# Kernel optimization log

Hardware: AMD Instinct MI355X
Metric: run time of the kernel (lower is better)

Reference implementation:

```python
import jax, jax.numpy as jnp
import numpy as np

K_ORDER, NUM_HEADS, BETA = 4, 2, 0.5
D_IN, D_OUT = 64, 64


def _batch_and_pos(n_nodes, N):
    # batch[i] = graph id of node i; pos[i] = index of node i within its graph
    batch = jnp.repeat(jnp.arange(n_nodes.shape[0], dtype=jnp.int32), n_nodes, total_repeat_length=N)
    ptr = jnp.concatenate([jnp.zeros(1, jnp.int32), jnp.cumsum(n_nodes).astype(jnp.int32)])
    pos = jnp.arange(N, dtype=jnp.int32) - ptr[batch]
    return batch, pos


def _to_pad(feat, batch, pos, Bsz, max_node):
    out_shape = (Bsz, max_node) + feat.shape[1:]
    return jnp.zeros(out_shape, feat.dtype).at[batch, pos].set(feat)


def fast_attn_conv(qs, ks, vs, n_nodes, batch, pos, max_node):
    # qs/ks/vs: [N,H,D]; linear attention with per-graph kv outer-product sums
    Bsz = n_nodes.shape[0]
    q_pad = _to_pad(qs, batch, pos, Bsz, max_node)  # [B,M,H,D]
    k_pad = _to_pad(ks, batch, pos, Bsz, max_node)
    v_pad = _to_pad(vs, batch, pos, Bsz, max_node)
    kv = jnp.einsum('bnhd,bnhe->bdhe', k_pad, v_pad)  # [B,D,H,D]
    v_sum = jax.ops.segment_sum(vs, batch, num_segments=Bsz)  # [B,H,D]
    k_sum = jax.ops.segment_sum(ks, batch, num_segments=Bsz)  # [B,H,D]
    numerator = jnp.einsum('bnhd,bdhe->bnhe', q_pad, kv)[batch, pos] + v_sum[batch]
    denom = jnp.einsum('bnhd,bhd->bnh', q_pad, k_sum)[batch, pos]
    denom = denom + n_nodes.astype(qs.dtype)[batch][:, None]
    return numerator / denom[..., None]


def gcn_conv(x, edge_index, e_feat):
    # x: [N,H,D], e_feat: [E,D]
    N = x.shape[0]
    row, col = edge_index[0], edge_index[1]
    deg = jax.ops.segment_sum(jnp.ones(row.shape[0], x.dtype), row, num_segments=N)
    dis = jnp.where(deg > 0, deg ** -0.5, jnp.zeros_like(deg))
    w = dis[row] * dis[col]  # [E]
    msg_edge = jax.ops.segment_sum(w[:, None] * e_feat, row, num_segments=N)  # [N,D]
    new_feat = jax.ops.segment_sum(x[col] * w[:, None, None], row, num_segments=N)  # [N,H,D]
    return new_feat + msg_edge[:, None, :]


def setup_inputs():
    key = jax.random.key(0)
    ks = jax.random.split(key, 10)
    B = 64
    n_nodes_np = np.tile(np.array([1000, 2000], np.int32), B // 2)  # sums to 96000
    N = int(n_nodes_np.sum())
    E = 768000
    x = jax.random.normal(ks[0], (N, D_IN), jnp.float32)
    edge_index = jax.random.randint(ks[1], (2, E), 0, N, jnp.int32)
    edge_attr = jax.random.randint(ks[2], (E, 3), 0, 8, jnp.int32)
    s = 0.02
    Wq_w = jax.random.normal(ks[3], (D_IN * NUM_HEADS, D_IN), jnp.float32) * s
    Wq_b = jnp.zeros((D_IN * NUM_HEADS,), jnp.float32)
    Wk_w = jax.random.normal(ks[4], (D_IN * NUM_HEADS, D_IN), jnp.float32) * s
    Wk_b = jnp.zeros((D_IN * NUM_HEADS,), jnp.float32)
    Wo_w = jax.random.normal(ks[5], (D_OUT, D_IN * NUM_HEADS), jnp.float32) * s
    Wo_b = jnp.zeros((D_OUT,), jnp.float32)
    bond_emb = jax.random.normal(ks[6], (3, 8, D_OUT), jnp.float32) * s
    return {"x": x, "Wq_w": Wq_w, "Wq_b": Wq_b, "Wk_w": Wk_w, "Wk_b": Wk_b,
            "Wo_w": Wo_w, "Wo_b": Wo_b, "bond_emb": bond_emb,
            "edge_index": edge_index, "edge_attr": edge_attr,
            "n_nodes": jnp.asarray(n_nodes_np)}


def reference(x, Wq_w, Wq_b, Wk_w, Wk_b, Wo_w, Wo_b, bond_emb, edge_index, edge_attr, n_nodes):
    N = x.shape[0]
    max_node = 2000  # static max over n_nodes
    batch, pos = _batch_and_pos(n_nodes, N)
    query = (x @ Wq_w.T + Wq_b).reshape(N, NUM_HEADS, D_IN)
    key_t = (x @ Wk_w.T + Wk_b).reshape(N, NUM_HEADS, D_IN)
    qs = query / jnp.linalg.norm(query, axis=2, keepdims=True)
    kk = key_t / jnp.linalg.norm(key_t, axis=2, keepdims=True)
    # BondEncoder: sum of per-feature embeddings
    e_feat = bond_emb[0][edge_attr[:, 0]] + bond_emb[1][edge_attr[:, 1]] + bond_emb[2][edge_attr[:, 2]]
    h = jnp.broadcast_to(x[:, None, :], (N, NUM_HEADS, D_IN))
    acc = h
    cur = h
    for _ in range(K_ORDER):
        gcn_i = gcn_conv(cur, edge_index, e_feat)
        attn_i = fast_attn_conv(qs, kk, cur, n_nodes, batch, pos, max_node)
        cur = BETA * gcn_i + (1.0 - BETA) * attn_i
        acc = acc + cur
    out = acc.reshape(N, NUM_HEADS * D_IN)
    return (out @ Wo_w.T + Wo_b) / NUM_HEADS
```

## Files before the change

kernel.cpp:

```cpp
#include <hip/hip_runtime.h>
#include <hip/hip_bf16.h>


typedef __attribute__((ext_vector_type(8))) short bf16x8;
typedef __attribute__((ext_vector_type(4))) float f32x4v;

#define CHUNK 50

__device__ __forceinline__ float asf(unsigned int u) { union { unsigned int i; float f; } v; v.i = u; return v.f; }
__device__ __forceinline__ float b2f_u(unsigned short u) { return asf((unsigned int)u << 16); }
__device__ __forceinline__ unsigned short f2b_u(float f) {
    __hip_bfloat16 h = __float2bfloat16(f);
    union { __hip_bfloat16 h; unsigned short u; } v; v.h = h; return v.u;
}
__device__ __forceinline__ unsigned int pack2(float a, float b) {
    return (unsigned int)f2b_u(a) | ((unsigned int)f2b_u(b) << 16);
}
__device__ __forceinline__ float wave_reduce_sum(float v) {
    #pragma unroll
    for (int off = 32; off > 0; off >>= 1) v += __shfl_xor(v, off, 64);
    return v;
}

__global__ void k_ptr(const int* __restrict__ nn, int* __restrict__ ptr,
                      int* __restrict__ cptr, int* __restrict__ tptr, int B) {
    if (threadIdx.x == 0 && blockIdx.x == 0) {
        int s = 0, c = 0, t = 0; ptr[0] = 0; cptr[0] = 0; tptr[0] = 0;
        for (int i = 0; i < B; ++i) {
            s += nn[i]; ptr[i + 1] = s;
            c += (nn[i] + CHUNK - 1) / CHUNK; cptr[i + 1] = c;
            t += (nn[i] + 15) / 16; tptr[i + 1] = t;
        }
    }
}

__global__ void k_batch(const int* __restrict__ ptr, int* __restrict__ batch) {
    int b = blockIdx.x;
    int s = ptr[b], e = ptr[b + 1];
    for (int i = s + threadIdx.x; i < e; i += blockDim.x) batch[i] = b;
}

__global__ void k_wcvt(const float* __restrict__ Wq_w, const float* __restrict__ Wk_w,
                       const float* __restrict__ Wo_w, unsigned short* __restrict__ Wb) {
    int i = blockIdx.x * 256 + threadIdx.x;
    if (i < 24576) {
        float v = (i < 8192) ? Wq_w[i] : ((i < 16384) ? Wk_w[i - 8192] : Wo_w[i - 16384]);
        Wb[i] = f2b_u(v);
    }
}

__global__ __launch_bounds__(256) void k_qkm(
    const float* __restrict__ x, const unsigned short* __restrict__ Wb,
    const float* __restrict__ Wq_b, const float* __restrict__ Wk_b,
    unsigned short* __restrict__ q, unsigned short* __restrict__ kq,
    unsigned short* __restrict__ curA, int N)
{
    int w = threadIdx.x >> 6, l = threadIdx.x & 63;
    int six = l & 15, quad = l >> 4;
    int base = (blockIdx.x * 4 + w) * 16;
    if (base >= N) return;
    int n = base + six;
    int nc = min(n, N - 1);

    const float* xr = x + (size_t)nc * 64;
    float4 xa = *(const float4*)(xr + quad * 8);
    float4 xb = *(const float4*)(xr + quad * 8 + 4);
    float4 xc = *(const float4*)(xr + 32 + quad * 8);
    float4 xd = *(const float4*)(xr + 32 + quad * 8 + 4);
    union { bf16x8 v; unsigned int u[4]; } b0, b1;
    b0.u[0] = pack2(xa.x, xa.y); b0.u[1] = pack2(xa.z, xa.w);
    b0.u[2] = pack2(xb.x, xb.y); b0.u[3] = pack2(xb.z, xb.w);
    b1.u[0] = pack2(xc.x, xc.y); b1.u[1] = pack2(xc.z, xc.w);
    b1.u[2] = pack2(xd.x, xd.y); b1.u[3] = pack2(xd.z, xd.w);
    if (n < N) {
        unsigned short* cr = curA + (size_t)n * 128;
        *(uint4*)(cr + quad * 8)       = make_uint4(b0.u[0], b0.u[1], b0.u[2], b0.u[3]);
        *(uint4*)(cr + 32 + quad * 8)  = make_uint4(b1.u[0], b1.u[1], b1.u[2], b1.u[3]);
        *(uint4*)(cr + 64 + quad * 8)  = make_uint4(b0.u[0], b0.u[1], b0.u[2], b0.u[3]);
        *(uint4*)(cr + 96 + quad * 8)  = make_uint4(b1.u[0], b1.u[1], b1.u[2], b1.u[3]);
    }

    #pragma unroll
    for (int g = 0; g < 4; ++g) {
        f32x4v c[4];
        #pragma unroll
        for (int tt = 0; tt < 4; ++tt) {
            int t = g * 4 + tt;
            const unsigned short* wr = Wb + (size_t)(t * 16 + six) * 64;
            bf16x8 a0 = *(const bf16x8*)(wr + quad * 8);
            bf16x8 a1 = *(const bf16x8*)(wr + 32 + quad * 8);
            f32x4v cc = {0.f, 0.f, 0.f, 0.f};
            cc = __builtin_amdgcn_mfma_f32_16x16x32_bf16(a0, b0.v, cc, 0, 0, 0);
            cc = __builtin_amdgcn_mfma_f32_16x16x32_bf16(a1, b1.v, cc, 0, 0, 0);
            c[tt] = cc;
        }
        const float* bias = (g < 2) ? Wq_b : Wk_b;
        int cb = (g & 1) * 64 + quad * 4;
        float ss = 0.f;
        #pragma unroll
        for (int tt = 0; tt < 4; ++tt)
            #pragma unroll
            for (int r = 0; r < 4; ++r) {
                float v = c[tt][r] + bias[cb + tt * 16 + r];
                c[tt][r] = v;
                ss += v * v;
            }
        ss += __shfl_xor(ss, 16, 64);
        ss += __shfl_xor(ss, 32, 64);
        float sc = rsqrtf(ss);
        if (n < N) {
            unsigned short* dst = ((g < 2) ? q : kq) + (size_t)n * 128;
            #pragma unroll
            for (int tt = 0; tt < 4; ++tt) {
                unsigned int u0 = pack2(c[tt][0] * sc, c[tt][1] * sc);
                unsigned int u1 = pack2(c[tt][2] * sc, c[tt][3] * sc);
                *(uint2*)(dst + cb + tt * 16) = make_uint2(u0, u1);
            }
        }
    }
}

__global__ void k_deg(const int* __restrict__ row, int* __restrict__ deg,
                      int* __restrict__ slot, int E) {
    int e = blockIdx.x * 256 + threadIdx.x;
    if (e < E) slot[e] = atomicAdd(&deg[row[e]], 1);
}

__global__ void k_scan1(const int* __restrict__ deg, int* __restrict__ rowstart,
                        int* __restrict__ bsum, float* __restrict__ dis, int N) {
    __shared__ int sh[256];
    int t = threadIdx.x, n = blockIdx.x * 256 + t;
    int v = (n < N) ? deg[n] : 0;
    if (n < N) dis[n] = v > 0 ? rsqrtf((float)v) : 0.f;
    sh[t] = v; __syncthreads();
    #pragma unroll
    for (int off = 1; off < 256; off <<= 1) {
        int add = (t >= off) ? sh[t - off] : 0;
        __syncthreads();
        sh[t] += add;
        __syncthreads();
    }
    if (n < N) rowstart[n] = sh[t] - v;
    if (t == 255) bsum[blockIdx.x] = sh[255];
}

__global__ void k_scan2(int* __restrict__ bsum, int nb) {
    __shared__ int sh[512];
    __shared__ int carry;
    int t = threadIdx.x;
    if (t == 0) carry = 0;
    __syncthreads();
    for (int base = 0; base < nb; base += 512) {
        int idx = base + t;
        int v = (idx < nb) ? bsum[idx] : 0;
        sh[t] = v; __syncthreads();
        for (int off = 1; off < 512; off <<= 1) {
            int add = (t >= off) ? sh[t - off] : 0;
            __syncthreads();
            sh[t] += add;
            __syncthreads();
        }
        if (idx < nb) bsum[idx] = sh[t] - v + carry;
        __syncthreads();
        if (t == 0) carry += sh[511];
        __syncthreads();
    }
}

__global__ void k_scan3(int* __restrict__ rowstart, const int* __restrict__ bsum, int N, int E) {
    int n = blockIdx.x * 256 + threadIdx.x;
    if (n < N) rowstart[n] += bsum[blockIdx.x];
    if (n == 0) rowstart[N] = E;
}

__global__ void k_fill(const int* __restrict__ eidx, const float* __restrict__ dis,
                       const int* __restrict__ rowstart, const int* __restrict__ slot,
                       int4* __restrict__ csr_pack, const int* __restrict__ eattr, int E) {
    int e = blockIdx.x * 256 + threadIdx.x;
    if (e >= E) return;
    int r = eidx[e], c = eidx[E + e];
    float wv = dis[r] * dis[c];
    int a0 = eattr[e * 3 + 0], a1 = eattr[e * 3 + 1], a2 = eattr[e * 3 + 2];
    int idx = rowstart[r] + slot[e];
    int4 v;
    v.x = c;
    v.y = __float_as_int(wv);
    v.z = a0 | (a1 << 8) | (a2 << 16);
    v.w = 0;
    csr_pack[idx] = v;
}

__global__ __launch_bounds__(256) void k_msg(
    const int* __restrict__ rowstart, const int4* __restrict__ csr_pack,
    const float* __restrict__ bond, unsigned short* __restrict__ msgb, int N) {
    __shared__ float bl[1536];
    int t = threadIdx.x, w = t >> 6, l = t & 63;
    for (int i = t; i < 1536; i += 256) bl[i] = bond[i];
    __syncthreads();
    for (int n = blockIdx.x * 4 + w; n < N; n += gridDim.x * 4) {
        int s0 = rowstart[n], s1 = rowstart[n + 1];
        float m = 0.f;
        #pragma unroll 4
        for (int i = s0; i < s1; ++i) {
            int4 pk = csr_pack[i];
            float wv = __int_as_float(pk.y);
            int att = pk.z;
            m += wv * (bl[(att & 255) * 64 + l] + bl[(8 + ((att >> 8) & 255)) * 64 + l]
                     + bl[(16 + (att >> 16)) * 64 + l]);
        }
        msgb[(size_t)n * 64 + l] = f2b_u(m);
    }
}

__global__ __launch_bounds__(256) void k_ksump(
    const unsigned short* __restrict__ kq, const int* __restrict__ ptr,
    const int* __restrict__ cptr, float* __restrict__ partKS, int B)
{
    int cid = blockIdx.x;
    if (cid >= cptr[B]) return;
    int lo = 0, hi = B - 1;
    while (lo < hi) { int mid = (lo + hi + 1) >> 1; if (cptr[mid] <= cid) lo = mid; else hi = mid - 1; }
    int b = lo;
    int start = ptr[b] + (cid - cptr[b]) * CHUNK;
    int end = min(start + CHUNK, ptr[b + 1]);
    int t = threadIdx.x, r = t >> 7, col = t & 127;
    float a = 0.f;
    for (int n = start + r; n < end; n += 2)
        a += b2f_u(kq[(size_t)n * 128 + col]);
    __shared__ float sh[256];
    sh[t] = a;
    __syncthreads();
    if (t < 128) partKS[(size_t)cid * 128 + t] = sh[t] + sh[t + 128];
}

__global__ __launch_bounds__(128) void k_ksr(
    const float* __restrict__ partKS, const int* __restrict__ cptr,
    float* __restrict__ ksum, int B)
{
    int b = blockIdx.x, t = threadIdx.x;
    float s = 0.f;
    int c0 = cptr[b], c1 = cptr[b + 1];
    for (int c = c0; c < c1; ++c) s += partKS[(size_t)c * 128 + t];
    ksum[b * 128 + t] = s;
}

__global__ __launch_bounds__(256) void k_denom(
    const unsigned short* __restrict__ q, const float* __restrict__ ksum,
    const int* __restrict__ batch, const int* __restrict__ nn,
    float* __restrict__ denom, int N)
{
    int w = threadIdx.x >> 6, l = threadIdx.x & 63;
    int n = blockIdx.x * 4 + w;
    if (n >= N) return;
    int b = batch[n];
    float d0 = b2f_u(q[(size_t)n * 128 + l]) * ksum[b * 128 + l];
    float d1 = b2f_u(q[(size_t)n * 128 + 64 + l]) * ksum[b * 128 + 64 + l];
    d0 = wave_reduce_sum(d0);
    d1 = wave_reduce_sum(d1);
    if (l == 0) {
        float nf = (float)nn[b];
        denom[n * 2 + 0] = d0 + nf;
        denom[n * 2 + 1] = d1 + nf;
    }
}

__global__ __launch_bounds__(256) void k_kvp(
    const unsigned short* __restrict__ kq, const unsigned short* __restrict__ cur,
    const int* __restrict__ ptr, const int* __restrict__ cptr,
    unsigned short* __restrict__ partKV, float* __restrict__ partVS, int B)
{
    int cid = blockIdx.x;
    if (cid >= cptr[B]) return;
    int lo = 0, hi = B - 1;
    while (lo < hi) { int mid = (lo + hi + 1) >> 1; if (cptr[mid] <= cid) lo = mid; else hi = mid - 1; }
    int b = lo;
    int start = ptr[b] + (cid - cptr[b]) * CHUNK;
    int end = min(start + CHUNK, ptr[b + 1]);

    int w = threadIdx.x >> 6, l = threadIdx.x & 63;
    int h = w >> 1, dhalf = w & 1;
    int d0 = dhalf * 32 + (l & 7) * 4;
    int e0 = (l >> 3) * 8;
    float a[4][8], va[8];
    #pragma unroll
    for (int i = 0; i < 4; ++i)
        #pragma unroll
        for (int j = 0; j < 8; ++j) a[i][j] = 0.f;
    #pragma unroll
    for (int j = 0; j < 8; ++j) va[j] = 0.f;

    const unsigned short* kp = kq + (size_t)start * 128 + h * 64 + d0;
    const unsigned short* vp = cur + (size_t)start * 128 + h * 64 + e0;
    #pragma unroll 4
    for (int n = start; n < end; ++n) {
        uint2 ku = *(const uint2*)kp;
        uint4 vu = *(const uint4*)vp;
        kp += 128; vp += 128;
        float k0 = asf(ku.x << 16), k1 = asf(ku.x & 0xffff0000u);
        float k2 = asf(ku.y << 16), k3 = asf(ku.y & 0xffff0000u);
        float v[8];
        v[0] = asf(vu.x << 16); v[1] = asf(vu.x & 0xffff0000u);
        v[2] = asf(vu.y << 16); v[3] = asf(vu.y & 0xffff0000u);
        v[4] = asf(vu.z << 16); v[5] = asf(vu.z & 0xffff0000u);
        v[6] = asf(vu.w << 16); v[7] = asf(vu.w & 0xffff0000u);
        #pragma unroll
        for (int j = 0; j < 8; ++j) {
            a[0][j] += k0 * v[j]; a[1][j] += k1 * v[j];
            a[2][j] += k2 * v[j]; a[3][j] += k3 * v[j];
            va[j] += v[j];
        }
    }
    unsigned short* dst = partKV + (size_t)cid * 8192 + h * 4096;
    #pragma unroll
    for (int j = 0; j < 8; ++j) {
        uint2 s2 = make_uint2(pack2(a[0][j], a[1][j]), pack2(a[2][j], a[3][j]));
        *(uint2*)(dst + (e0 + j) * 64 + d0) = s2;
    }
    if (dhalf == 0 && (l & 7) == 0) {
        float* vdst = partVS + (size_t)cid * 128 + h * 64 + e0;
        #pragma unroll
        for (int j = 0; j < 8; ++j) vdst[j] = va[j];
    }
}

__global__ __launch_bounds__(256) void k_red(
    const unsigned short* __restrict__ partKV, const float* __restrict__ partVS,
    const int* __restrict__ cptr, unsigned short* __restrict__ kvT_b,
    float* __restrict__ vsum, int B)
{
    int bid = blockIdx.x;
    int gh = bid >> 1, half = bid & 1;
    int g = gh >> 1, h = gh & 1;
    int c0 = cptr[g], c1 = cptr[g + 1];
    int t = threadIdx.x;
    int off = half * 2048 + t * 8;
    float s[8];
    #pragma unroll
    for (int i = 0; i < 8; ++i) s[i] = 0.f;
    for (int c = c0; c < c1; ++c) {
        uint4 u = *(const uint4*)(partKV + (size_t)c * 8192 + h * 4096 + off);
        s[0] += asf(u.x << 16); s[1] += asf(u.x & 0xffff0000u);
        s[2] += asf(u.y << 16); s[3] += asf(u.y & 0xffff0000u);
        s[4] += asf(u.z << 16); s[5] += asf(u.z & 0xffff0000u);
        s[6] += asf(u.w << 16); s[7] += asf(u.w & 0xffff0000u);
    }
    unsigned int u[4];
    #pragma unroll
    for (int i = 0; i < 4; ++i) u[i] = pack2(s[2 * i], s[2 * i + 1]);
    *(uint4*)(kvT_b + (size_t)gh * 4096 + off) = make_uint4(u[0], u[1], u[2], u[3]);
    if (half == 0 && t < 64) {
        float vs = 0.f;
        for (int c = c0; c < c1; ++c) vs += partVS[(size_t)c * 128 + h * 64 + t];
        vsum[g * 128 + h * 64 + t] = vs;
    }
}

__global__ __launch_bounds__(256) void k_attn(
    const unsigned short* __restrict__ q, const unsigned short* __restrict__ kvT,
    const float* __restrict__ vsum, const float* __restrict__ denom,
    const int* __restrict__ ptr, const int* __restrict__ tptr,
    const unsigned short* __restrict__ msgb,
    unsigned short* __restrict__ curB, int B)
{
    int w = threadIdx.x >> 6, l = threadIdx.x & 63;
    int tid = blockIdx.x * 4 + w;
    if (tid >= tptr[B]) return;
    int lo = 0, hi = B - 1;
    while (lo < hi) { int mid = (lo + hi + 1) >> 1; if (tptr[mid] <= tid) lo = mid; else hi = mid - 1; }
    int b0 = lo;
    int start = ptr[b0] + (tid - tptr[b0]) * 16;
    int end = min(start + 16, ptr[b0 + 1]);
    int quad = l >> 4, six = l & 15;
    int n = start + six;
    int nc = min(n, end - 1);
    bool live = n < end;
    const unsigned short* mrow = msgb + (size_t)nc * 64;
    uint2 me[4];
    #pragma unroll
    for (int et = 0; et < 4; ++et) me[et] = *(const uint2*)(mrow + et * 16 + quad * 4);
    #pragma unroll
    for (int h = 0; h < 2; ++h) {
        const unsigned short* qrow = q + (size_t)nc * 128 + h * 64;
        bf16x8 qb0 = *(const bf16x8*)(qrow + quad * 8);
        bf16x8 qb1 = *(const bf16x8*)(qrow + 32 + quad * 8);
        const unsigned short* Bb = kvT + (size_t)(b0 * 2 + h) * 4096;
        float dn = denom[nc * 2 + h];
        const float* vsb = vsum + (b0 * 2 + h) * 64;
        #pragma unroll
        for (int et = 0; et < 4; ++et) {
            const unsigned short* arow = Bb + (size_t)(et * 16 + six) * 64;
            bf16x8 a0 = *(const bf16x8*)(arow + quad * 8);
            bf16x8 a1 = *(const bf16x8*)(arow + 32 + quad * 8);
            f32x4v c = {0.f, 0.f, 0.f, 0.f};
            c = __builtin_amdgcn_mfma_f32_16x16x32_bf16(a0, qb0, c, 0, 0, 0);
            c = __builtin_amdgcn_mfma_f32_16x16x32_bf16(a1, qb1, c, 0, 0, 0);
            float4 vs = *(const float4*)(vsb + et * 16 + quad * 4);
            float m0 = asf(me[et].x << 16), m1 = asf(me[et].x & 0xffff0000u);
            float m2 = asf(me[et].y << 16), m3 = asf(me[et].y & 0xffff0000u);
            float v0 = 0.5f * (c[0] + vs.x) / dn + 0.5f * m0;
            float v1 = 0.5f * (c[1] + vs.y) / dn + 0.5f * m1;
            float v2 = 0.5f * (c[2] + vs.z) / dn + 0.5f * m2;
            float v3 = 0.5f * (c[3] + vs.w) / dn + 0.5f * m3;
            if (live) {
                uint2 st = make_uint2(pack2(v0, v1), pack2(v2, v3));
                *(uint2*)(curB + (size_t)n * 128 + h * 64 + et * 16 + quad * 4) = st;
            }
        }
    }
}

__global__ __launch_bounds__(256) void k_gcn(
    const unsigned short* __restrict__ curA,
    const int* __restrict__ rowstart, const int4* __restrict__ csr_pack,
    unsigned short* __restrict__ curB, unsigned short* __restrict__ acc, int N, int first)
{
    int orig = blockIdx.x, nwg = gridDim.x;
    int q8 = nwg >> 3, r8 = nwg & 7;
    int xcd = orig & 7, jj = orig >> 3;
    int swz = (xcd < r8 ? xcd * (q8 + 1) : r8 * (q8 + 1) + (xcd - r8) * q8) + jj;

    int w = threadIdx.x >> 6, l = threadIdx.x & 63;
    int qq = l >> 4, ql = l & 15;
    int half = qq >> 1;
    int par  = qq & 1;
    int nA = swz * 8 + w * 2;
    if (nA >= N) return;
    bool hasB = (nA + 1) < N;
    int myN = nA + half;
    bool live = myN < N;
    int s0  = rowstart[nA];
    int sA1 = rowstart[nA + 1];
    int s1  = hasB ? rowstart[nA + 2] : sA1;
    int base = half ? sA1 : s0;
    int lim  = half ? s1  : sA1;

    int e0 = 8 * ql + par * 4;
    size_t o = (size_t)myN * 128 + e0;
    const unsigned short* accsrc = first ? curA : acc;
    uint2 ub = make_uint2(0, 0), ua = make_uint2(0, 0);
    if (live) {
        ub = *(const uint2*)(curB + o);
        ua = *(const uint2*)(accsrc + o);
    }

    float g[8];
    #pragma unroll
    for (int j = 0; j < 8; ++j) g[j] = 0.f;
    const int2* cw2 = (const int2*)csr_pack;
    #pragma unroll 2
    for (int i = base + par; i < lim; i += 2) {
        int2 cw = cw2[2 * i];
        float wv = __int_as_float(cw.y);
        uint4 u = *(const uint4*)(curA + (size_t)cw.x * 128 + 8 * ql);
        g[0] += wv * asf(u.x << 16); g[1] += wv * asf(u.x & 0xffff0000u);
        g[2] += wv * asf(u.y << 16); g[3] += wv * asf(u.y & 0xffff0000u);
        g[4] += wv * asf(u.z << 16); g[5] += wv * asf(u.z & 0xffff0000u);
        g[6] += wv * asf(u.w << 16); g[7] += wv * asf(u.w & 0xffff0000u);
    }
    #pragma unroll
    for (int j = 0; j < 8; ++j) g[j] += __shfl_xor(g[j], 16, 64);
    float s0v = par ? g[4] : g[0];
    float s1v = par ? g[5] : g[1];
    float s2v = par ? g[6] : g[2];
    float s3v = par ? g[7] : g[3];
    if (live) {
        float v0 = 0.5f * s0v + asf(ub.x << 16);
        float v1 = 0.5f * s1v + asf(ub.x & 0xffff0000u);
        float v2 = 0.5f * s2v + asf(ub.y << 16);
        float v3 = 0.5f * s3v + asf(ub.y & 0xffff0000u);
        *(uint2*)(curB + o) = make_uint2(pack2(v0, v1), pack2(v2, v3));
        float a0 = asf(ua.x << 16) + v0, a1 = asf(ua.x & 0xffff0000u) + v1;
        float a2 = asf(ua.y << 16) + v2, a3 = asf(ua.y & 0xffff0000u) + v3;
        *(uint2*)(acc + o) = make_uint2(pack2(a0, a1), pack2(a2, a3));
    }
}

__global__ __launch_bounds__(256) void k_outm(
    const unsigned short* __restrict__ acc, const unsigned short* __restrict__ Wob,
    const float* __restrict__ Wo_b, float* __restrict__ out, int N)
{
    int w = threadIdx.x >> 6, l = threadIdx.x & 63;
    int six = l & 15, quad = l >> 4;
    int base = (blockIdx.x * 4 + w) * 16;
    if (base >= N) return;
    int n = base + six;
    int nc = min(n, N - 1);
    const unsigned short* ar = acc + (size_t)nc * 128;
    bf16x8 b0 = *(const bf16x8*)(ar + quad * 8);
    bf16x8 b1 = *(const bf16x8*)(ar + 32 + quad * 8);
    bf16x8 b2 = *(const bf16x8*)(ar + 64 + quad * 8);
    bf16x8 b3 = *(const bf16x8*)(ar + 96 + quad * 8);
    #pragma unroll
    for (int t = 0; t < 4; ++t) {
        const unsigned short* wr = Wob + (size_t)(t * 16 + six) * 128;
        bf16x8 a0 = *(const bf16x8*)(wr + quad * 8);
        bf16x8 a1 = *(const bf16x8*)(wr + 32 + quad * 8);
        bf16x8 a2 = *(const bf16x8*)(wr + 64 + quad * 8);
        bf16x8 a3 = *(const bf16x8*)(wr + 96 + quad * 8);
        f32x4v c = {0.f, 0.f, 0.f, 0.f};
        c = __builtin_amdgcn_mfma_f32_16x16x32_bf16(a0, b0, c, 0, 0, 0);
        c = __builtin_amdgcn_mfma_f32_16x16x32_bf16(a1, b1, c, 0, 0, 0);
        c = __builtin_amdgcn_mfma_f32_16x16x32_bf16(a2, b2, c, 0, 0, 0);
        c = __builtin_amdgcn_mfma_f32_16x16x32_bf16(a3, b3, c, 0, 0, 0);
        if (n < N) {
            float4 bias = *(const float4*)(Wo_b + t * 16 + quad * 4);
            float4 o4;
            o4.x = (c[0] + bias.x) * 0.5f;
            o4.y = (c[1] + bias.y) * 0.5f;
            o4.z = (c[2] + bias.z) * 0.5f;
            o4.w = (c[3] + bias.w) * 0.5f;
            *(float4*)(out + (size_t)n * 64 + t * 16 + quad * 4) = o4;
        }
    }
}

extern "C" void kernel_launch(void* const* d_in, const int* in_sizes, int n_in,
                              void* d_out, int out_size, void* d_ws, size_t ws_size,
                              hipStream_t stream) {
    const float* x    = (const float*)d_in[0];
    const float* Wq_w = (const float*)d_in[1];
    const float* Wq_b = (const float*)d_in[2];
    const float* Wk_w = (const float*)d_in[3];
    const float* Wk_b = (const float*)d_in[4];
    const float* Wo_w = (const float*)d_in[5];
    const float* Wo_b = (const float*)d_in[6];
    const float* bond = (const float*)d_in[7];
    const int*   eidx = (const int*)d_in[8];
    const int*   eattr= (const int*)d_in[9];
    const int*   nn   = (const int*)d_in[10];
    float* out = (float*)d_out;
    int N = in_sizes[0] / 64;
    int E = in_sizes[9] / 3;
    int B = in_sizes[10];

    char* p = (char*)d_ws;
    auto alloc = [&](size_t bytes) { char* r = p; p += (bytes + 255) & ~(size_t)255; return r; };
    unsigned short* q    = (unsigned short*)alloc((size_t)N * 128 * 2);
    unsigned short* kq   = (unsigned short*)alloc((size_t)N * 128 * 2);
    unsigned short* curA = (unsigned short*)alloc((size_t)N * 128 * 2);
    unsigned short* curB = (unsigned short*)alloc((size_t)N * 128 * 2);
    unsigned short* acc  = (unsigned short*)alloc((size_t)N * 128 * 2);
    int maxchunks = (N + CHUNK - 1) / CHUNK + B;
    int maxtiles  = (N + 15) / 16 + B;
    unsigned short* partKV = (unsigned short*)alloc((size_t)maxchunks * 8192 * 2);
    float* partVS = (float*)alloc((size_t)maxchunks * 128 * 4);
    float* partKS = (float*)alloc((size_t)maxchunks * 128 * 4);
    unsigned short* kvT_b = (unsigned short*)alloc((size_t)B * 2 * 64 * 64 * 2);
    float* vsum  = (float*)alloc((size_t)B * 128 * 4);
    float* ksum  = (float*)alloc((size_t)B * 128 * 4);
    float* denom = (float*)alloc((size_t)N * 2 * 4);
    float* dis   = (float*)alloc((size_t)N * 4);
    int* deg     = (int*)alloc((size_t)N * 4);
    int* rowstart= (int*)alloc((size_t)(N + 1) * 4);
    int* slot    = (int*)alloc((size_t)E * 4);
    int4* csr_pack = (int4*)alloc((size_t)E * 16);
    int* batch   = (int*)alloc((size_t)N * 4);
    int* ptr     = (int*)alloc((size_t)(B + 1) * 4);
    int* cptr    = (int*)alloc((size_t)(B + 1) * 4);
    int* tptr    = (int*)alloc((size_t)(B + 1) * 4);
    unsigned short* Wb = (unsigned short*)alloc(24576 * 2);
    int nb = (N + 255) / 256;
    int* bsum    = (int*)alloc((size_t)nb * 4);
    unsigned short* msgb = (unsigned short*)out;

    hipMemsetAsync(deg, 0, (size_t)N * 4, stream);

    k_ptr  <<<1, 64, 0, stream>>>(nn, ptr, cptr, tptr, B);
    k_batch<<<B, 256, 0, stream>>>(ptr, batch);
    k_wcvt <<<96, 256, 0, stream>>>(Wq_w, Wk_w, Wo_w, Wb);
    k_qkm  <<<(N + 63) / 64, 256, 0, stream>>>(x, Wb, Wq_b, Wk_b, q, kq, curA, N);
    k_deg  <<<(E + 255) / 256, 256, 0, stream>>>(eidx, deg, slot, E);
    k_scan1<<<nb, 256, 0, stream>>>(deg, rowstart, bsum, dis, N);
    k_scan2<<<1, 512, 0, stream>>>(bsum, nb);
    k_scan3<<<nb, 256, 0, stream>>>(rowstart, bsum, N, E);
    k_fill <<<(E + 255) / 256, 256, 0, stream>>>(eidx, dis, rowstart, slot, csr_pack, eattr, E);
    k_msg  <<<2048, 256, 0, stream>>>(rowstart, csr_pack, bond, msgb, N);
    k_ksump<<<maxchunks, 256, 0, stream>>>(kq, ptr, cptr, partKS, B);
    k_ksr  <<<B, 128, 0, stream>>>(partKS, cptr, ksum, B);
    k_denom<<<(N + 3) / 4, 256, 0, stream>>>(q, ksum, batch, nn, denom, N);

    int gcnblk = (N + 7) / 8;
    for (int it = 0; it < 4; ++it) {
        k_kvp <<<maxchunks, 256, 0, stream>>>(kq, curA, ptr, cptr, partKV, partVS, B);
        k_red <<<B * 4, 256, 0, stream>>>(partKV, partVS, cptr, kvT_b, vsum, B);
        k_attn<<<(maxtiles + 3) / 4, 256, 0, stream>>>(q, kvT_b, vsum, denom, ptr, tptr, msgb, curB, B);
        k_gcn <<<gcnblk, 256, 0, stream>>>(curA, rowstart, csr_pack, curB, acc, N, it == 0 ? 1 : 0);
        unsigned short* tmp = curA; curA = curB; curB = tmp;
    }
    k_outm<<<(N + 63) / 64, 256, 0, stream>>>(acc, Wb + 16384, Wo_b, out, N);
}
```

Before: 808.1 us.

## Compute per-chunk KV outer products with MFMA and enlarge chunk size

Rewrites the per-chunk K^T V partial-sum kernel to use bf16 MFMA 16x16x32 instructions instead of scalar FMA loops, with the V row sums obtained from an extra MFMA against a ones vector. The chunk size rises from 50 to 128 nodes, so there are fewer partial blocks and less reduction work, at the cost of fewer blocks in flight. The loads become scalar strided bf16 gathers with tail masking, and the partial results are written with scalar 16-bit stores. A separate small change loads the projection bias as float4.

```diff
diff --git a/kernel.cpp b/kernel.cpp
--- a/kernel.cpp
+++ b/kernel.cpp
@@ -5,7 +5,7 @@
 typedef __attribute__((ext_vector_type(8))) short bf16x8;
 typedef __attribute__((ext_vector_type(4))) float f32x4v;
 
-#define CHUNK 50
+#define CHUNK 128
 
 __device__ __forceinline__ float asf(unsigned int u) { union { unsigned int i; float f; } v; v.i = u; return v.f; }
 __device__ __forceinline__ float b2f_u(unsigned short u) { return asf((unsigned int)u << 16); }
@@ -98,13 +98,12 @@
         int cb = (g & 1) * 64 + quad * 4;
         float ss = 0.f;
         #pragma unroll
-        for (int tt = 0; tt < 4; ++tt)
-            #pragma unroll
-            for (int r = 0; r < 4; ++r) {
-                float v = c[tt][r] + bias[cb + tt * 16 + r];
-                c[tt][r] = v;
-                ss += v * v;
-            }
+        for (int tt = 0; tt < 4; ++tt) {
+            float4 bv = *(const float4*)(bias + cb + tt * 16);
+            c[tt][0] += bv.x; c[tt][1] += bv.y; c[tt][2] += bv.z; c[tt][3] += bv.w;
+            ss += c[tt][0] * c[tt][0] + c[tt][1] * c[tt][1]
+                + c[tt][2] * c[tt][2] + c[tt][3] * c[tt][3];
+        }
         ss += __shfl_xor(ss, 16, 64);
         ss += __shfl_xor(ss, 32, 64);
         float sc = rsqrtf(ss);
@@ -279,47 +278,83 @@
 
     int w = threadIdx.x >> 6, l = threadIdx.x & 63;
     int h = w >> 1, dhalf = w & 1;
-    int d0 = dhalf * 32 + (l & 7) * 4;
-    int e0 = (l >> 3) * 8;
-    float a[4][8], va[8];
-    #pragma unroll
-    for (int i = 0; i < 4; ++i)
+    int six = l & 15, quad = l >> 4;
+
+    f32x4v c00 = {0,0,0,0}, c01 = {0,0,0,0}, c10 = {0,0,0,0}, c11 = {0,0,0,0};
+    f32x4v c20 = {0,0,0,0}, c21 = {0,0,0,0}, c30 = {0,0,0,0}, c31 = {0,0,0,0};
+    f32x4v s0 = {0,0,0,0}, s1 = {0,0,0,0}, s2 = {0,0,0,0}, s3 = {0,0,0,0};
+
+    const unsigned short ONE = 0x3F80;
+
+    for (int nb = start; nb < end; nb += 32) {
+        union { bf16x8 v; unsigned short s[8]; } a0u, a1u, a2u, a3u, b0u, b1u, onu;
+        if (nb + 32 <= end) {
+            const unsigned short* vb = cur + (size_t)(nb + quad * 8) * 128 + h * 64 + six;
+            const unsigned short* kb = kq  + (size_t)(nb + quad * 8) * 128 + h * 64 + dhalf * 32 + six;
+            #pragma unroll
+            for (int j = 0; j < 8; ++j) {
+                a0u.s[j] = vb[j * 128];
+                a1u.s[j] = vb[j * 128 + 16];
+                a2u.s[j] = vb[j * 128 + 32];
+                a3u.s[j] = vb[j * 128 + 48];
+                b0u.s[j] = kb[j * 128];
+                b1u.s[j] = kb[j * 128 + 16];
+                onu.s[j] = ONE;
+            }
+        } else {
+            #pragma unroll
+            for (int j = 0; j < 8; ++j) {
+                int nd = nb + quad * 8 + j;
+                int ndc = min(nd, end - 1);
+                bool ok = nd < end;
+                const unsigned short* vb = cur + (size_t)ndc * 128 + h * 64 + six;
+                const unsigned short* kb = kq  + (size_t)ndc * 128 + h * 64 + dhalf * 32 + six;
+                a0u.s[j] = vb[0];
+                a1u.s[j] = vb[16];
+                a2u.s[j] = vb[32];
+                a3u.s[j] = vb[48];
+                b0u.s[j] = ok ? kb[0]  : (unsigned short)0;
+                b1u.s[j] = ok ? kb[16] : (unsigned short)0;
+                onu.s[j] = ok ? ONE : (unsigned short)0;
+            }
+        }
+        c00 = __builtin_amdgcn_mfma_f32_16x16x32_bf16(a0u.v, b0u.v, c00, 0, 0, 0);
+        c01 = __builtin_amdgcn_mfma_f32_16x16x32_bf16(a0u.v, b1u.v, c01, 0, 0, 0);
+        c10 = __builtin_amdgcn_mfma_f32_16x16x32_bf16(a1u.v, b0u.v, c10, 0, 0, 0);
+        c11 = __builtin_amdgcn_mfma_f32_16x16x32_bf16(a1u.v, b1u.v, c11, 0, 0, 0);
+        c20 = __builtin_amdgcn_mfma_f32_16x16x32_bf16(a2u.v, b0u.v, c20, 0, 0, 0);
+        c21 = __builtin_amdgcn_mfma_f32_16x16x32_bf16(a2u.v, b1u.v, c21, 0, 0, 0);
+        c30 = __builtin_amdgcn_mfma_f32_16x16x32_bf16(a3u.v, b0u.v, c30, 0, 0, 0);
+        c31 = __builtin_amdgcn_mfma_f32_16x16x32_bf16(a3u.v, b1u.v, c31, 0, 0, 0);
+        s0  = __builtin_amdgcn_mfma_f32_16x16x32_bf16(a0u.v, onu.v, s0, 0, 0, 0);
+        s1  = __builtin_amdgcn_mfma_f32_16x16x32_bf16(a1u.v, onu.v, s1, 0, 0, 0);
+        s2  = __builtin_amdgcn_mfma_f32_16x16x32_bf16(a2u.v, onu.v, s2, 0, 0, 0);
+        s3  = __builtin_amdgcn_mfma_f32_16x16x32_bf16(a3u.v, onu.v, s3, 0, 0, 0);
+    }
+
+    unsigned short* dst = partKV + (size_t)cid * 8192 + h * 4096 + dhalf * 32 + six;
+    #pragma unroll
+    for (int r = 0; r < 4; ++r) {
+        int e = quad * 4 + r;
+        dst[(e +  0) * 64 +  0] = f2b_u(c00[r]);
+        dst[(e +  0) * 64 + 16] = f2b_u(c01[r]);
+        dst[(e + 16) * 64 +  0] = f2b_u(c10[r]);
+        dst[(e + 16) * 64 + 16] = f2b_u(c11[r]);
+        dst[(e + 32) * 64 +  0] = f2b_u(c20[r]);
+        dst[(e + 32) * 64 + 16] = f2b_u(c21[r]);
+        dst[(e + 48) * 64 +  0] = f2b_u(c30[r]);
+        dst[(e + 48) * 64 + 16] = f2b_u(c31[r]);
+    }
+    if (dhalf == 0 && six == 0) {
+        float* vdst = partVS + (size_t)cid * 128 + h * 64;
         #pragma unroll
-        for (int j = 0; j < 8; ++j) a[i][j] = 0.f;
-    #pragma unroll
-    for (int j = 0; j < 8; ++j) va[j] = 0.f;
-
-    const unsigned short* kp = kq + (size_t)start * 128 + h * 64 + d0;
-    const unsigned short* vp = cur + (size_t)start * 128 + h * 64 + e0;
-    #pragma unroll 4
-    for (int n = start; n < end; ++n) {
-        uint2 ku = *(const uint2*)kp;
-        uint4 vu = *(const uint4*)vp;
-        kp += 128; vp += 128;
-        float k0 = asf(ku.x << 16), k1 = asf(ku.x & 0xffff0000u);
-        float k2 = asf(ku.y << 16), k3 = asf(ku.y & 0xffff0000u);
-        float v[8];
-        v[0] = asf(vu.x << 16); v[1] = asf(vu.x & 0xffff0000u);
-        v[2] = asf(vu.y << 16); v[3] = asf(vu.y & 0xffff0000u);
-        v[4] = asf(vu.z << 16); v[5] = asf(vu.z & 0xffff0000u);
-        v[6] = asf(vu.w << 16); v[7] = asf(vu.w & 0xffff0000u);
-        #pragma unroll
-        for (int j = 0; j < 8; ++j) {
-            a[0][j] += k0 * v[j]; a[1][j] += k1 * v[j];
-            a[2][j] += k2 * v[j]; a[3][j] += k3 * v[j];
-            va[j] += v[j];
-        }
-    }
-    unsigned short* dst = partKV + (size_t)cid * 8192 + h * 4096;
-    #pragma unroll
-    for (int j = 0; j < 8; ++j) {
-        uint2 s2 = make_uint2(pack2(a[0][j], a[1][j]), pack2(a[2][j], a[3][j]));
-        *(uint2*)(dst + (e0 + j) * 64 + d0) = s2;
-    }
-    if (dhalf == 0 && (l & 7) == 0) {
-        float* vdst = partVS + (size_t)cid * 128 + h * 64 + e0;
-        #pragma unroll
-        for (int j = 0; j < 8; ++j) vdst[j] = va[j];
+        for (int r = 0; r < 4; ++r) {
+            int e = quad * 4 + r;
+            vdst[e]      = s0[r];
+            vdst[e + 16] = s1[r];
+            vdst[e + 32] = s2[r];
+            vdst[e + 48] = s3[r];
+        }
     }
 }
 
```

New measurement: 671.0 us. 1.2x faster.
